# Kernel optimization log

Hardware: AMD Instinct MI355X
Metric: run time of the kernel (lower is better)

Reference implementation:

```python
import jax, jax.numpy as jnp
import numpy as np

D = 1024
H = 16
HD = D // H
T = 2048
B = 2
EPS = 1e-7

def setup_inputs() -> dict:
    key = jax.random.key(0)
    ks = jax.random.split(key, 16)
    s = 0.02
    return {
        "x":  jax.random.normal(ks[0], (B, T, D), jnp.float32),
        "Wq": jax.random.normal(ks[1], (D, D), jnp.float32) * s,
        "bq": jnp.zeros((D,), jnp.float32),
        "Wk": jax.random.normal(ks[2], (D, D), jnp.float32) * s,
        "bk": jnp.zeros((D,), jnp.float32),
        "Wv": jax.random.normal(ks[3], (D, D), jnp.float32) * s,
        "bv": jnp.zeros((D,), jnp.float32),
        "Wo": jax.random.normal(ks[4], (D, D), jnp.float32) * s,
        "bo": jnp.zeros((D,), jnp.float32),
        "W1": jax.random.normal(ks[5], (D, 4 * D), jnp.float32) * s,
        "b1": jnp.zeros((4 * D,), jnp.float32),
        "W2": jax.random.normal(ks[6], (4 * D, D), jnp.float32) * s,
        "b2": jnp.zeros((D,), jnp.float32),
        "g1": jnp.ones((D,), jnp.float32),
        "be1": jnp.zeros((D,), jnp.float32),
        "g2": jnp.ones((D,), jnp.float32),
        "be2": jnp.zeros((D,), jnp.float32),
    }

def layer_norm(x, gamma, beta):
    mu = jnp.mean(x, axis=-1, keepdims=True)
    var = jnp.mean(jnp.square(x - mu), axis=-1, keepdims=True)  # biased var
    return (x - mu) / jnp.sqrt(var + EPS) * gamma + beta

def attention(x, Wq, bq, Wk, bk, Wv, bv, Wo, bo):
    b, t, d = x.shape
    q = (x @ Wq + bq).reshape(b, t, H, HD).transpose(0, 2, 1, 3)  # [B,H,T,HD]
    k = (x @ Wk + bk).reshape(b, t, H, HD).transpose(0, 2, 1, 3)
    v = (x @ Wv + bv).reshape(b, t, H, HD).transpose(0, 2, 1, 3)
    scores = jnp.einsum("bhqd,bhkd->bhqk", q, k) / np.sqrt(HD).astype(np.float32)
    causal = jnp.tril(jnp.ones((t, t), bool))
    scores = jnp.where(causal, scores, -jnp.inf)
    attn = jax.nn.softmax(scores, axis=-1)
    out = jnp.einsum("bhqk,bhkd->bhqd", attn, v)
    out = out.transpose(0, 2, 1, 3).reshape(b, t, d)
    return out @ Wo + bo

def reference(x, Wq, bq, Wk, bk, Wv, bv, Wo, bo, W1, b1, W2, b2, g1, be1, g2, be2):
    x = x + attention(layer_norm(x, g1, be1), Wq, bq, Wk, bk, Wv, bv, Wo, bo)
    h = layer_norm(x, g2, be2)
    x = x + (jax.nn.relu(h @ W1 + b1) @ W2 + b2)
    return x
```

## Files before the change

### kernel.cpp

```cpp
#include <hip/hip_runtime.h>
#include <hip/hip_bf16.h>

#define Dm 1024
#define Hn 16
#define HDm 64
#define Tm 2048
#define Bm 2
#define MR (Bm*Tm)
#define SQK 3072

typedef __attribute__((ext_vector_type(8))) short bfrag8;
typedef __attribute__((ext_vector_type(4))) float floatx4;

__device__ __forceinline__ float bf2f(ushort u){
  union { unsigned int i; float f; } c; c.i = ((unsigned int)u)<<16; return c.f;
}
__device__ __forceinline__ ushort f2bf(float f){
  unsigned int u = __float_as_uint(f);
  u += 0x7fffu + ((u>>16)&1u);
  return (ushort)(u>>16);
}
__device__ __forceinline__ void gl2lds16(const ushort* g, ushort* l){
  __builtin_amdgcn_global_load_lds(
    (const __attribute__((address_space(1))) unsigned int*)g,
    (__attribute__((address_space(3))) unsigned int*)l,
    16, 0, 0);
}
__device__ __forceinline__ int is_f32(const unsigned int* g1w){
  return *g1w == 0x3F800000u;
}

__global__ __launch_bounds__(256) void prep_vec(const void* bq, const void* bk, const void* bv,
                                                const void* bo, const void* b1, const void* b2,
                                                const void* g1, const void* be1,
                                                const void* g2, const void* be2,
                                                float* __restrict__ dst){
  int i = blockIdx.x*256 + threadIdx.x;
  if (i >= 13312) return;
  int f = is_f32((const unsigned int*)g1);
  const void* src; int off;
  if      (i < 1024)  { src = bq;  off = i; }
  else if (i < 2048)  { src = bk;  off = i-1024; }
  else if (i < 3072)  { src = bv;  off = i-2048; }
  else if (i < 4096)  { src = bo;  off = i-3072; }
  else if (i < 8192)  { src = b1;  off = i-4096; }
  else if (i < 9216)  { src = b2;  off = i-8192; }
  else if (i < 10240) { src = g1;  off = i-9216; }
  else if (i < 11264) { src = be1; off = i-10240; }
  else if (i < 12288) { src = g2;  off = i-11264; }
  else                { src = be2; off = i-12288; }
  dst[i] = f ? ((const float*)src)[off] : bf2f(((const ushort*)src)[off]);
}

__device__ __forceinline__ void transpose_body(const void* src, ushort* dst,
                                               int K, int N, int f32){
  __shared__ ushort s[32][33];
  int bx = blockIdx.x, by = blockIdx.y;
  int tx = threadIdx.x, ty = threadIdx.y;
#pragma unroll
  for(int r=0;r<4;r++){
    size_t gi = (size_t)(by*32+ty+8*r)*N + bx*32+tx;
    s[ty+8*r][tx] = f32 ? f2bf(((const float*)src)[gi]) : ((const ushort*)src)[gi];
  }
  __syncthreads();
#pragma unroll
  for(int r=0;r<4;r++)
    dst[(size_t)(bx*32+ty+8*r)*K + by*32+tx] = s[tx][ty+8*r];
}
__global__ __launch_bounds__(256) void transpose_cast(const void* __restrict__ src,
                                                      ushort* __restrict__ dst,
                                                      int K, int N, const unsigned int* g1w){
  transpose_body(src, dst, K, N, is_f32(g1w));
}
__global__ __launch_bounds__(256) void transpose_qkvo(const void* Wq, const void* Wk,
                                                      const void* Wv, const void* Wo,
                                                      ushort* __restrict__ Wqkvt,
                                                      ushort* __restrict__ Wot,
                                                      const unsigned int* g1w){
  int z = blockIdx.z;
  const void* src = (z==0)?Wq:(z==1)?Wk:(z==2)?Wv:Wo;
  ushort* dst = (z<3) ? (Wqkvt + (size_t)z*1024*1024) : Wot;
  transpose_body(src, dst, 1024, 1024, is_f32(g1w));
}

__global__ __launch_bounds__(256) void vtrans(const ushort* __restrict__ qkv,
                                              ushort* __restrict__ vt){
  __shared__ ushort s[32][33];
  int bhz = blockIdx.z;
  int bx = blockIdx.x;
  int by = blockIdx.y;
  int tx = threadIdx.x, ty = threadIdx.y;
  int b = bhz>>4, h = bhz&15;
  const ushort* src = qkv + (size_t)b*Tm*SQK + 2048 + h*64;
#pragma unroll
  for(int r=0;r<4;r++)
    s[ty+8*r][tx] = src[(size_t)(bx*32+ty+8*r)*SQK + by*32+tx];
  __syncthreads();
  ushort* dst = vt + (size_t)bhz*HDm*Tm;
#pragma unroll
  for(int r=0;r<4;r++)
    dst[(size_t)(by*32+ty+8*r)*Tm + bx*32+tx] = s[tx][ty+8*r];
}

template<int MODE>
__global__ __launch_bounds__(256) void ln_kernel(const void* __restrict__ xin,
                                                 const float* __restrict__ g,
                                                 const float* __restrict__ be,
                                                 ushort* __restrict__ out,
                                                 const unsigned int* g1w){
  int row = blockIdx.x;
  int tid = threadIdx.x;
  size_t base = (size_t)row*Dm + tid*4;
  float v[4];
  bool f32in = (MODE==1) || (MODE==0 && is_f32(g1w));
  if (f32in){
    const float4 t = *(const float4*)((const float*)xin + base);
    v[0]=t.x; v[1]=t.y; v[2]=t.z; v[3]=t.w;
  } else {
    ushort4 t = *(const ushort4*)((const ushort*)xin + base);
    v[0]=bf2f(t.x); v[1]=bf2f(t.y); v[2]=bf2f(t.z); v[3]=bf2f(t.w);
  }
  float s  = v[0]+v[1]+v[2]+v[3];
  float s2 = v[0]*v[0]+v[1]*v[1]+v[2]*v[2]+v[3]*v[3];
#pragma unroll
  for(int o=1;o<64;o<<=1){
    s  += __shfl_xor(s,  o, 64);
    s2 += __shfl_xor(s2, o, 64);
  }
  __shared__ float red[8];
  int wv = tid>>6;
  if ((tid&63)==0){ red[wv]=s; red[wv+4]=s2; }
  __syncthreads();
  s  = red[0]+red[1]+red[2]+red[3];
  s2 = red[4]+red[5]+red[6]+red[7];
  float mu  = s  * (1.0f/Dm);
  float var = s2 * (1.0f/Dm) - mu*mu;
  float rstd = rsqrtf(var + 1e-7f);
  float4 gg = *(const float4*)(g  + tid*4);
  float4 bb = *(const float4*)(be + tid*4);
  ushort4 o4;
  o4.x = f2bf((v[0]-mu)*rstd*gg.x+bb.x);
  o4.y = f2bf((v[1]-mu)*rstd*gg.y+bb.y);
  o4.z = f2bf((v[2]-mu)*rstd*gg.z+bb.z);
  o4.w = f2bf((v[3]-mu)*rstd*gg.w+bb.w);
  *(ushort4*)(out + base) = o4;
}

#define BMt 128
#define BKt 64

enum { E_BF16=0, E_RELU=1, E_OPROJ=2, E_FINALB=3 };

template<int EPI, int BN>
__global__ __launch_bounds__(256) void gemm_bt(const ushort* __restrict__ A, int lda,
                                               const ushort* __restrict__ Bt, int ldb,
                                               const float* __restrict__ bias,
                                               const void*   __restrict__ resid,
                                               void* __restrict__ Cout, int ldc,
                                               int Ki,
                                               const unsigned int* g1w){
  constexpr int JN = BN/32;
  __shared__ ushort As[BMt*BKt];
  __shared__ ushort Bs[BN*BKt];
  int tid = threadIdx.x;
  int bn = blockIdx.x, bm = blockIdx.y;
  int wv = tid>>6, lane = tid&63;
  int quad = lane>>4, l16 = lane&15;
  int wm = (wv&1)*64, wn = (wv>>1)*(BN/2);
  floatx4 acc[4][JN] = {};
  const ushort* Aptr = A  + (size_t)bm*BMt*lda;
  const ushort* Bptr = Bt + (size_t)bn*BN*ldb;
  int rl = lane>>3;
  int cs = ((lane&7) ^ rl)*8;

  for(int k0=0; k0<Ki; k0+=BKt){
    __syncthreads();
#pragma unroll
    for(int c=0;c<4;c++)
      gl2lds16(&Aptr[(size_t)(wv*32 + c*8 + rl)*lda + k0 + cs], &As[(wv*32 + c*8)*BKt]);
    if (BN == 128){
#pragma unroll
      for(int c=0;c<4;c++)
        gl2lds16(&Bptr[(size_t)(wv*32 + c*8 + rl)*ldb + k0 + cs], &Bs[(wv*32 + c*8)*BKt]);
    } else {
#pragma unroll
      for(int c=0;c<2;c++)
        gl2lds16(&Bptr[(size_t)(wv*16 + c*8 + rl)*ldb + k0 + cs], &Bs[(wv*16 + c*8)*BKt]);
    }
    __syncthreads();
#pragma unroll
    for(int f=0;f<2;f++){
      int sw = (((f<<2)|quad) ^ (l16&7))*8;
      bfrag8 a[4], b[JN];
#pragma unroll
      for(int i=0;i<4;i++) a[i] = *(const bfrag8*)&As[(wm+i*16+l16)*BKt + sw];
#pragma unroll
      for(int j=0;j<JN;j++) b[j] = *(const bfrag8*)&Bs[(wn+j*16+l16)*BKt + sw];
#pragma unroll
      for(int i=0;i<4;i++)
#pragma unroll
        for(int j=0;j<JN;j++)
          acc[i][j] = __builtin_amdgcn_mfma_f32_16x16x32_bf16(a[i], b[j], acc[i][j], 0,0,0);
    }
  }

  int f32 = 0;
  if (EPI==E_OPROJ || EPI==E_FINALB) f32 = is_f32(g1w);
#pragma unroll
  for(int i=0;i<4;i++){
    int gr = bm*BMt + wm + i*16 + quad*4;
#pragma unroll
    for(int j=0;j<JN;j++){
      int gc = bn*BN + wn + j*16 + l16;
      float bb = bias ? bias[gc] : 0.0f;
#pragma unroll
      for(int rg=0; rg<4; rg++){
        size_t idx = (size_t)(gr+rg)*ldc + gc;
        float val = acc[i][j][rg] + bb;
        if (EPI==E_BF16){
          ((ushort*)Cout)[idx] = f2bf(val);
        } else if (EPI==E_RELU){
          ((ushort*)Cout)[idx] = f2bf(val>0.0f?val:0.0f);
        } else if (EPI==E_OPROJ){
          float r = f32 ? ((const float*)resid)[idx] : bf2f(((const ushort*)resid)[idx]);
          ((ushort*)Cout)[idx] = f2bf(val + r);
        } else {
          float r = bf2f(((const ushort*)resid)[idx]);
          if (f32) ((float*)Cout)[idx] = val + r;
          else     ((ushort*)Cout)[idx] = f2bf(val + r);
        }
      }
    }
  }
}

#define PSTR 72

__global__ __launch_bounds__(256) void attn_mfma(const ushort* __restrict__ qkv,
                                                 const ushort* __restrict__ vt,
                                                 ushort* __restrict__ out){
  __shared__ ushort Ks[64*64];
  __shared__ ushort Vs[64*64];
  __shared__ ushort Ps[64*PSTR];
  int bxp = blockIdx.x, h = blockIdx.y, b = blockIdx.z;
  int tid = threadIdx.x;
  int wv = tid>>6, lane = tid&63;
  int quad = lane>>4, l16 = lane&15;
  const ushort* qbase = qkv + (size_t)b*Tm*SQK + h*HDm;
  const ushort* kbase = qbase + Dm;
  const ushort* vtb   = vt + (size_t)(b*Hn+h)*HDm*Tm;
  size_t obase = (size_t)b*Tm*Dm + (size_t)h*HDm;
  int rl = lane>>3;
  int cs = ((lane&7) ^ rl)*8;

  for(int half=0; half<2; half++){
    int qt = half ? (31 - bxp) : bxp;
    int qrow = qt*64 + wv*16 + l16;
    bfrag8 aq[2];
#pragma unroll
    for(int f=0;f<2;f++){
      bfrag8 raw = *(const bfrag8*)&qbase[(size_t)qrow*SQK + f*32 + quad*8];
#pragma unroll
      for(int e=0;e<8;e++) aq[f][e] = (short)f2bf(bf2f((ushort)raw[e])*0.125f);
    }

    floatx4 oacc[4] = {};
    float lacc[4] = {0.0f,0.0f,0.0f,0.0f};

    for(int kt=0; kt<=qt; kt++){
      __syncthreads();
#pragma unroll
      for(int c=0;c<2;c++){
        int r = wv*16 + c*8;
        gl2lds16(&kbase[(size_t)(kt*64 + r + rl)*SQK + cs], &Ks[r*64]);
        gl2lds16(&vtb[(size_t)(r + rl)*Tm + kt*64 + cs],    &Vs[r*64]);
      }
      __syncthreads();

      floatx4 s[4];
#pragma unroll
      for(int j=0;j<4;j++){
        int row = j*16+l16;
        bfrag8 b0 = *(const bfrag8*)&Ks[row*64 + ((quad     ^ (l16&7))*8)];
        bfrag8 b1 = *(const bfrag8*)&Ks[row*64 + (((4|quad) ^ (l16&7))*8)];
        floatx4 z = {0.0f,0.0f,0.0f,0.0f};
        z = __builtin_amdgcn_mfma_f32_16x16x32_bf16(aq[0], b0, z, 0,0,0);
        z = __builtin_amdgcn_mfma_f32_16x16x32_bf16(aq[1], b1, z, 0,0,0);
        s[j] = z;
      }
      if (kt==qt){
#pragma unroll
        for(int j=0;j<4;j++)
#pragma unroll
          for(int rg=0;rg<4;rg++)
            if ((j*16+l16) > (wv*16+quad*4+rg)) s[j][rg] = -1.0e30f;
      }

      ushort pb[4][4];
#pragma unroll
      for(int j=0;j<4;j++)
#pragma unroll
        for(int rg=0;rg<4;rg++){
          float p = __expf(s[j][rg]);
          lacc[rg] += p;
          pb[j][rg] = f2bf(p);
        }

#pragma unroll
      for(int j=0;j<4;j++)
#pragma unroll
        for(int rg=0;rg<4;rg++)
          Ps[(wv*16 + quad*4+rg)*PSTR + j*16 + l16] = pb[j][rg];

      bfrag8 ap0 = *(const bfrag8*)&Ps[(wv*16 + l16)*PSTR +      quad*8];
      bfrag8 ap1 = *(const bfrag8*)&Ps[(wv*16 + l16)*PSTR + 32 + quad*8];
#pragma unroll
      for(int j=0;j<4;j++){
        int row = j*16+l16;
        bfrag8 bv0 = *(const bfrag8*)&Vs[row*64 + ((quad     ^ (l16&7))*8)];
        bfrag8 bv1 = *(const bfrag8*)&Vs[row*64 + (((4|quad) ^ (l16&7))*8)];
        oacc[j] = __builtin_amdgcn_mfma_f32_16x16x32_bf16(ap0, bv0, oacc[j], 0,0,0);
        oacc[j] = __builtin_amdgcn_mfma_f32_16x16x32_bf16(ap1, bv1, oacc[j], 0,0,0);
      }
    }

#pragma unroll
    for(int o=1;o<16;o<<=1)
#pragma unroll
      for(int rg=0;rg<4;rg++) lacc[rg] += __shfl_xor(lacc[rg], o, 64);
    float inv[4];
#pragma unroll
    for(int rg=0;rg<4;rg++) inv[rg] = 1.0f / lacc[rg];

#pragma unroll
    for(int j=0;j<4;j++)
#pragma unroll
      for(int rg=0;rg<4;rg++){
        int t = qt*64 + wv*16 + quad*4 + rg;
        out[obase + (size_t)t*Dm + j*16 + l16] = f2bf(oacc[j][rg] * inv[rg]);
      }
  }
}

extern "C" void kernel_launch(void* const* d_in, const int* in_sizes, int n_in,
                              void* d_out, int out_size, void* d_ws, size_t ws_size,
                              hipStream_t stream) {
  const void* x   = d_in[0];
  const void* Wq  = d_in[1];
  const void* bq  = d_in[2];
  const void* Wk  = d_in[3];
  const void* bk  = d_in[4];
  const void* Wv  = d_in[5];
  const void* bv  = d_in[6];
  const void* Wo  = d_in[7];
  const void* bo  = d_in[8];
  const void* W1  = d_in[9];
  const void* b1  = d_in[10];
  const void* W2  = d_in[11];
  const void* b2  = d_in[12];
  const void* g1  = d_in[13];
  const void* be1 = d_in[14];
  const void* g2  = d_in[15];
  const void* be2 = d_in[16];
  const unsigned int* g1w = (const unsigned int*)g1;

  char* ws = (char*)d_ws;
  const size_t MB = 1024*1024;
  float*  biasf = (float*)(ws + 65536);
  ushort* Wqkvt = (ushort*)(ws + 1*MB);
  ushort* Wot   = (ushort*)(ws + 7*MB);
  ushort* W1t   = (ushort*)(ws + 9*MB);
  ushort* W2t   = (ushort*)(ws + 17*MB);
  ushort* ln1   = (ushort*)(ws + 25*MB);
  ushort* vtb   = (ushort*)(ws + 25*MB);
  ushort* h2    = (ushort*)(ws + 25*MB);
  ushort* qkv   = (ushort*)(ws + 33*MB);
  ushort* atb   = (ushort*)(ws + 57*MB);
  ushort* x1b   = (ushort*)(ws + 65*MB);
  ushort* h1    = (ushort*)(ws + 33*MB);

  prep_vec<<<52, 256, 0, stream>>>(bq,bk,bv,bo,b1,b2,g1,be1,g2,be2, biasf);

  dim3 tb(32,8);
  transpose_qkvo<<<dim3(32,32,4), tb, 0, stream>>>(Wq, Wk, Wv, Wo, Wqkvt, Wot, g1w);
  transpose_cast<<<dim3(128,32), tb, 0, stream>>>(W1, W1t, 1024, 4096, g1w);
  transpose_cast<<<dim3(32,128), tb, 0, stream>>>(W2, W2t, 4096, 1024, g1w);

  ln_kernel<0><<<MR, 256, 0, stream>>>(x, biasf+9216, biasf+10240, ln1, g1w);

  gemm_bt<E_BF16,128><<<dim3(24,32), 256, 0, stream>>>(ln1, 1024, Wqkvt, 1024, biasf, nullptr, qkv, SQK, 1024, g1w);

  vtrans<<<dim3(64,2,32), tb, 0, stream>>>(qkv, vtb);

  attn_mfma<<<dim3(16, Hn, Bm), 256, 0, stream>>>(qkv, vtb, atb);

  gemm_bt<E_OPROJ,64><<<dim3(16,32), 256, 0, stream>>>(atb, 1024, Wot, 1024, biasf+3072, x, x1b, 1024, 1024, g1w);

  ln_kernel<2><<<MR, 256, 0, stream>>>(x1b, biasf+11264, biasf+12288, h2, g1w);

  gemm_bt<E_RELU,128><<<dim3(32,32), 256, 0, stream>>>(h2, 1024, W1t, 1024, biasf+4096, nullptr, h1, 4096, 1024, g1w);
  gemm_bt<E_FINALB,64><<<dim3(16,32), 256, 0, stream>>>(h1, 4096, W2t, 4096, biasf+8192, x1b, d_out, 1024, 4096, g1w);
}
```

Baseline: 388.1 us.

## Use 64x64 tiles with XCD-aware block mapping for N=1024 GEMMs and attention

Adds a gemm64_bt kernel that uses 64x64 output tiles and 128 threads for the O-projection and the second FFN GEMM. The grid grows from 512 to 1024 blocks, which gives better occupancy across the CUs. Those GEMMs and the attention kernel now use a 1D grid whose block IDs are remapped so that blocks on the same XCD share A rows or heads, aiming for better L2 reuse. The trade-off is that smaller tiles give lower arithmetic intensity per block and reload more operand data.

New measurement: 377.0 us. 2.8% less time.

```diff
diff --git a/kernel.cpp b/kernel.cpp
--- a/kernel.cpp
+++ b/kernel.cpp
@@ -146,12 +146,10 @@
   *(ushort4*)(out + base) = o4;
 }
 
-#define BMt 128
 #define BKt 64
-
 enum { E_BF16=0, E_RELU=1, E_OPROJ=2, E_FINALB=3 };
 
-template<int EPI, int BN>
+template<int EPI>
 __global__ __launch_bounds__(256) void gemm_bt(const ushort* __restrict__ A, int lda,
                                                const ushort* __restrict__ Bt, int ldb,
                                                const float* __restrict__ bias,
@@ -159,69 +157,121 @@
                                                void* __restrict__ Cout, int ldc,
                                                int Ki,
                                                const unsigned int* g1w){
-  constexpr int JN = BN/32;
-  __shared__ ushort As[BMt*BKt];
-  __shared__ ushort Bs[BN*BKt];
+  __shared__ ushort As[128*BKt];
+  __shared__ ushort Bs[128*BKt];
   int tid = threadIdx.x;
   int bn = blockIdx.x, bm = blockIdx.y;
   int wv = tid>>6, lane = tid&63;
   int quad = lane>>4, l16 = lane&15;
-  int wm = (wv&1)*64, wn = (wv>>1)*(BN/2);
-  floatx4 acc[4][JN] = {};
-  const ushort* Aptr = A  + (size_t)bm*BMt*lda;
-  const ushort* Bptr = Bt + (size_t)bn*BN*ldb;
+  int wm = (wv&1)*64, wn = (wv>>1)*64;
+  floatx4 acc[4][4] = {};
+  const ushort* Aptr = A  + (size_t)bm*128*lda;
+  const ushort* Bptr = Bt + (size_t)bn*128*ldb;
   int rl = lane>>3;
   int cs = ((lane&7) ^ rl)*8;
 
   for(int k0=0; k0<Ki; k0+=BKt){
     __syncthreads();
 #pragma unroll
-    for(int c=0;c<4;c++)
+    for(int c=0;c<4;c++){
       gl2lds16(&Aptr[(size_t)(wv*32 + c*8 + rl)*lda + k0 + cs], &As[(wv*32 + c*8)*BKt]);
-    if (BN == 128){
-#pragma unroll
-      for(int c=0;c<4;c++)
-        gl2lds16(&Bptr[(size_t)(wv*32 + c*8 + rl)*ldb + k0 + cs], &Bs[(wv*32 + c*8)*BKt]);
-    } else {
-#pragma unroll
-      for(int c=0;c<2;c++)
-        gl2lds16(&Bptr[(size_t)(wv*16 + c*8 + rl)*ldb + k0 + cs], &Bs[(wv*16 + c*8)*BKt]);
+      gl2lds16(&Bptr[(size_t)(wv*32 + c*8 + rl)*ldb + k0 + cs], &Bs[(wv*32 + c*8)*BKt]);
     }
     __syncthreads();
 #pragma unroll
     for(int f=0;f<2;f++){
       int sw = (((f<<2)|quad) ^ (l16&7))*8;
-      bfrag8 a[4], b[JN];
+      bfrag8 a[4], b[4];
 #pragma unroll
       for(int i=0;i<4;i++) a[i] = *(const bfrag8*)&As[(wm+i*16+l16)*BKt + sw];
 #pragma unroll
-      for(int j=0;j<JN;j++) b[j] = *(const bfrag8*)&Bs[(wn+j*16+l16)*BKt + sw];
+      for(int j=0;j<4;j++) b[j] = *(const bfrag8*)&Bs[(wn+j*16+l16)*BKt + sw];
 #pragma unroll
       for(int i=0;i<4;i++)
 #pragma unroll
-        for(int j=0;j<JN;j++)
+        for(int j=0;j<4;j++)
           acc[i][j] = __builtin_amdgcn_mfma_f32_16x16x32_bf16(a[i], b[j], acc[i][j], 0,0,0);
     }
   }
 
-  int f32 = 0;
-  if (EPI==E_OPROJ || EPI==E_FINALB) f32 = is_f32(g1w);
 #pragma unroll
   for(int i=0;i<4;i++){
-    int gr = bm*BMt + wm + i*16 + quad*4;
-#pragma unroll
-    for(int j=0;j<JN;j++){
-      int gc = bn*BN + wn + j*16 + l16;
+    int gr = bm*128 + wm + i*16 + quad*4;
+#pragma unroll
+    for(int j=0;j<4;j++){
+      int gc = bn*128 + wn + j*16 + l16;
       float bb = bias ? bias[gc] : 0.0f;
 #pragma unroll
       for(int rg=0; rg<4; rg++){
         size_t idx = (size_t)(gr+rg)*ldc + gc;
         float val = acc[i][j][rg] + bb;
-        if (EPI==E_BF16){
-          ((ushort*)Cout)[idx] = f2bf(val);
-        } else if (EPI==E_RELU){
-          ((ushort*)Cout)[idx] = f2bf(val>0.0f?val:0.0f);
-        } else if (EPI==E_OPROJ){
+        if (EPI==E_BF16)      ((ushort*)Cout)[idx] = f2bf(val);
+        else      ((ushort*)Cout)[idx] = f2bf(val>0.0f?val:0.0f);
+      }
+    }
+  }
+}
+
+template<int EPI>
+__global__ __launch_bounds__(128) void gemm64_bt(const ushort* __restrict__ A, int lda,
+                                                 const ushort* __restrict__ Bt, int ldb,
+                                                 const float* __restrict__ bias,
+                                                 const void*   __restrict__ resid,
+                                                 void* __restrict__ Cout, int ldc,
+                                                 int Ki,
+                                                 const unsigned int* g1w){
+  __shared__ ushort As[64*BKt];
+  __shared__ ushort Bs[64*BKt];
+  int tid = threadIdx.x;
+  int id = blockIdx.x;
+  int xcd = id&7, sdec = id>>3;
+  int bn = sdec&15, bm = (sdec>>4)*8 + xcd;
+  int wv = tid>>6, lane = tid&63;
+  int quad = lane>>4, l16 = lane&15;
+  int wm = wv*32;
+  floatx4 acc[2][4] = {};
+  const ushort* Aptr = A  + (size_t)bm*64*lda;
+  const ushort* Bptr = Bt + (size_t)bn*64*ldb;
+  int rl = lane>>3;
+  int cs = ((lane&7) ^ rl)*8;
+
+  for(int k0=0; k0<Ki; k0+=BKt){
+    __syncthreads();
+#pragma unroll
+    for(int c=0;c<4;c++){
+      gl2lds16(&Aptr[(size_t)(wv*32 + c*8 + rl)*lda + k0 + cs], &As[(wv*32 + c*8)*BKt]);
+      gl2lds16(&Bptr[(size_t)(wv*32 + c*8 + rl)*ldb + k0 + cs], &Bs[(wv*32 + c*8)*BKt]);
+    }
+    __syncthreads();
+#pragma unroll
+    for(int f=0;f<2;f++){
+      int sw = (((f<<2)|quad) ^ (l16&7))*8;
+      bfrag8 a[2], b[4];
+#pragma unroll
+      for(int i=0;i<2;i++) a[i] = *(const bfrag8*)&As[(wm+i*16+l16)*BKt + sw];
+#pragma unroll
+      for(int j=0;j<4;j++) b[j] = *(const bfrag8*)&Bs[(j*16+l16)*BKt + sw];
+#pragma unroll
+      for(int i=0;i<2;i++)
+#pragma unroll
+        for(int j=0;j<4;j++)
+          acc[i][j] = __builtin_amdgcn_mfma_f32_16x16x32_bf16(a[i], b[j], acc[i][j], 0,0,0);
+    }
+  }
+
+  int f32 = is_f32(g1w);
+#pragma unroll
+  for(int i=0;i<2;i++){
+    int gr = bm*64 + wm + i*16 + quad*4;
+#pragma unroll
+    for(int j=0;j<4;j++){
+      int gc = bn*64 + j*16 + l16;
+      float bb = bias[gc];
+#pragma unroll
+      for(int rg=0; rg<4; rg++){
+        size_t idx = (size_t)(gr+rg)*ldc + gc;
+        float val = acc[i][j][rg] + bb;
+        if (EPI==E_OPROJ){
           float r = f32 ? ((const float*)resid)[idx] : bf2f(((const ushort*)resid)[idx]);
           ((ushort*)Cout)[idx] = f2bf(val + r);
         } else {
@@ -242,7 +292,10 @@
   __shared__ ushort Ks[64*64];
   __shared__ ushort Vs[64*64];
   __shared__ ushort Ps[64*PSTR];
-  int bxp = blockIdx.x, h = blockIdx.y, b = blockIdx.z;
+  int id = blockIdx.x;
+  int xcd = id&7, sdec = id>>3;
+  int bxp = sdec&15, hb = sdec>>4;
+  int h = xcd + 8*(hb&1), b = hb>>1;
   int tid = threadIdx.x;
   int wv = tid>>6, lane = tid&63;
   int quad = lane>>4, l16 = lane&15;
@@ -388,16 +441,16 @@
 
   ln_kernel<0><<<MR, 256, 0, stream>>>(x, biasf+9216, biasf+10240, ln1, g1w);
 
-  gemm_bt<E_BF16,128><<<dim3(24,32), 256, 0, stream>>>(ln1, 1024, Wqkvt, 1024, biasf, nullptr, qkv, SQK, 1024, g1w);
+  gemm_bt<E_BF16><<<dim3(24,32), 256, 0, stream>>>(ln1, 1024, Wqkvt, 1024, biasf, nullptr, qkv, SQK, 1024, g1w);
 
   vtrans<<<dim3(64,2,32), tb, 0, stream>>>(qkv, vtb);
 
-  attn_mfma<<<dim3(16, Hn, Bm), 256, 0, stream>>>(qkv, vtb, atb);
-
-  gemm_bt<E_OPROJ,64><<<dim3(16,32), 256, 0, stream>>>(atb, 1024, Wot, 1024, biasf+3072, x, x1b, 1024, 1024, g1w);
+  attn_mfma<<<512, 256, 0, stream>>>(qkv, vtb, atb);
+
+  gemm64_bt<E_OPROJ><<<1024, 128, 0, stream>>>(atb, 1024, Wot, 1024, biasf+3072, x, x1b, 1024, 1024, g1w);
 
   ln_kernel<2><<<MR, 256, 0, stream>>>(x1b, biasf+11264, biasf+12288, h2, g1w);
 
-  gemm_bt<E_RELU,128><<<dim3(32,32), 256, 0, stream>>>(h2, 1024, W1t, 1024, biasf+4096, nullptr, h1, 4096, 1024, g1w);
-  gemm_bt<E_FINALB,64><<<dim3(16,32), 256, 0, stream>>>(h1, 4096, W2t, 4096, biasf+8192, x1b, d_out, 1024, 4096, g1w);
-}
+  gemm_bt<E_RELU><<<dim3(32,32), 256, 0, stream>>>(h2, 1024, W1t, 1024, biasf+4096, nullptr, h1, 4096, 1024, g1w);
+  gemm64_bt<E_FINALB><<<1024, 128, 0, stream>>>(h1, 4096, W2t, 4096, biasf+8192, x1b, d_out, 1024, 4096, g1w);
+}
```
